# Kernel optimization log

Hardware: AMD Instinct MI355X
Metric: run time of the kernel (lower is better)

The kernel has to match this reference:

```python
import math
import jax, jax.numpy as jnp
import numpy as np

HEAD = 16
DIM = 1024
DH = DIM // HEAD
NEG = -100000000.0


def setup_inputs() -> dict:
    key = jax.random.key(0)
    ks = jax.random.split(key, 12)
    B, S, D = 2, 2048, DIM
    s = 1.0 / math.sqrt(D)
    return {
        "key": jax.random.normal(ks[0], (B, S, D), jnp.float32),
        "value": jax.random.normal(ks[1], (B, S, D), jnp.float32),
        "query": jax.random.normal(ks[2], (B, S, D), jnp.float32),
        "mask": jax.random.randint(ks[3], (B, 1, S, S), 0, 2) == 1,
        "Wq": jax.random.normal(ks[4], (D, D), jnp.float32) * s,
        "bq": jnp.zeros((D,), jnp.float32),
        "Wk": jax.random.normal(ks[5], (D, D), jnp.float32) * s,
        "bk": jnp.zeros((D,), jnp.float32),
        "Wv": jax.random.normal(ks[6], (D, D), jnp.float32) * s,
        "bv": jnp.zeros((D,), jnp.float32),
        "Wo": jax.random.normal(ks[7], (D, D), jnp.float32) * s,
        "bo": jnp.zeros((D,), jnp.float32),
    }


def _split_heads(x, b):
    # [B, S, D] -> [B, H, S, Dh]
    return x.reshape(b, -1, HEAD, DH).transpose(0, 2, 1, 3)


def reference(key, value, query, mask, Wq, bq, Wk, bk, Wv, bv, Wo, bo):
    b, k_len, d = key.shape
    q_len = query.shape[1]
    k_up = _split_heads(key @ Wk.T + bk, b)
    v_up = _split_heads(value @ Wv.T + bv, b)
    q_up = _split_heads(query @ Wq.T + bq, b) / math.sqrt(DH)
    scores = jnp.einsum("bhqd,bhkd->bhqk", q_up, k_up)
    scores = jnp.where(mask, NEG, scores)
    attn = jax.nn.softmax(scores, axis=-1)
    # dropout is identity in eval/reference mode
    context = jnp.einsum("bhqk,bhkd->bhqd", attn, v_up)
    context = context.transpose(0, 2, 1, 3).reshape(b, q_len, d)
    out = context @ Wo.T + bo
    return out, attn
```

## Files before the change

### kernel.cpp

```cpp
#include <hip/hip_runtime.h>
#include <stdint.h>

#define S_LEN 2048
#define D_MODEL 1024
#define N_HEAD 16
#define D_HEAD 64
#define N_BATCH 2
#define M_TOK (N_BATCH * S_LEN)

typedef unsigned short u16;
typedef unsigned int u32;
typedef __attribute__((ext_vector_type(8))) short bf16x8;
typedef __attribute__((ext_vector_type(4))) short s16x4;
typedef __attribute__((ext_vector_type(4))) float f32x4;
typedef __attribute__((ext_vector_type(4))) unsigned short u16x4;

#define MFMA16(a, b, c) __builtin_amdgcn_mfma_f32_16x16x32_bf16((a), (b), (c), 0, 0, 0)

#if defined(__has_builtin)
#if __has_builtin(__builtin_amdgcn_mfma_f32_16x16x16bf16_1k)
#define HAVE_MFMA_16x16x16 1
#define MFMA_PV(a, b, c) __builtin_amdgcn_mfma_f32_16x16x16bf16_1k((a), (b), (c), 0, 0, 0)
#endif
#endif

#define WAITCNT(n) asm volatile("s_waitcnt vmcnt(" #n ")" ::: "memory")
#define BAR() __builtin_amdgcn_s_barrier()

__device__ __forceinline__ u16 f2bf(float f) {
  unsigned int u = __float_as_uint(f);
  u = (u + 0x7FFFu + ((u >> 16) & 1u)) >> 16;
  return (u16)u;
}

__device__ __forceinline__ void gload_lds16(const u16* g, u16* l) {
  __builtin_amdgcn_global_load_lds((const __attribute__((address_space(1))) void*)g,
                                   (__attribute__((address_space(3))) void*)l, 16, 0, 0);
}

#define N4BIG (M_TOK * D_MODEL / 4)
#define N4W (D_MODEL * D_MODEL / 4)
__global__ __launch_bounds__(256) void cvt7_kernel(
    const float* __restrict__ sk, const float* __restrict__ sv, const float* __restrict__ sq,
    const float* __restrict__ swq, const float* __restrict__ swk, const float* __restrict__ swv,
    const float* __restrict__ swo, u16* __restrict__ dk, u16* __restrict__ dv, u16* __restrict__ dq,
    u16* __restrict__ dwq, u16* __restrict__ dwk, u16* __restrict__ dwv, u16* __restrict__ dwo) {
  const float* s;
  u16* d;
  int n4;
  switch (blockIdx.y) {
    case 0: s = sk; d = dk; n4 = N4BIG; break;
    case 1: s = sv; d = dv; n4 = N4BIG; break;
    case 2: s = sq; d = dq; n4 = N4BIG; break;
    case 3: s = swq; d = dwq; n4 = N4W; break;
    case 4: s = swk; d = dwk; n4 = N4W; break;
    case 5: s = swv; d = dwv; n4 = N4W; break;
    default: s = swo; d = dwo; n4 = N4W; break;
  }
  int i = blockIdx.x * blockDim.x + threadIdx.x;
  int stride = gridDim.x * blockDim.x;
  for (; i < n4; i += stride) {
    float4 v = ((const float4*)s)[i];
    u16x4 o = {f2bf(v.x), f2bf(v.y), f2bf(v.z), f2bf(v.w)};
    ((u16x4*)d)[i] = o;
  }
}

__global__ __launch_bounds__(256) void pack_mask(const int* __restrict__ mask,
                                                 unsigned long long* __restrict__ packed) {
  int wid = (blockIdx.x * blockDim.x + threadIdx.x) >> 6;
  int lane = threadIdx.x & 63;
  int nw = (gridDim.x * blockDim.x) >> 6;
  const int NW64 = M_TOK * (S_LEN / 64);
  for (int widx = wid; widx < NW64; widx += nw) {
    int m = mask[(size_t)widx * 64 + lane];
    unsigned long long bits = __ballot(m != 0);
    if (lane == 0) packed[widx] = bits;
  }
}

__device__ __forceinline__ void gemm_body(const u16* __restrict__ A, const u16* __restrict__ Bw,
                                          const float* __restrict__ bias, void* __restrict__ Cout,
                                          float scale, int outmode) {
  __shared__ u16 As[128 * 32];
  __shared__ u16 Bs[128 * 32];
  const int K = D_MODEL, N = D_MODEL;
  int tid = threadIdx.x;
  int w = tid >> 6, lane = tid & 63, lg = lane >> 4, lr = lane & 15;
  int m0 = blockIdx.x * 128, n0 = blockIdx.y * 128;
  int wr = w >> 1, wc = w & 1;
  f32x4 acc[4][4] = {};
  int r0 = tid >> 2;
  int r1 = 64 + (tid >> 2);
  int kk0 = (tid & 3) * 8;
  for (int kb = 0; kb < K; kb += 32) {
    gload_lds16(A + (size_t)(m0 + r0) * K + kb + kk0, As + w * 512);
    gload_lds16(A + (size_t)(m0 + r1) * K + kb + kk0, As + 2048 + w * 512);
    gload_lds16(Bw + (size_t)(n0 + r0) * K + kb + kk0, Bs + w * 512);
    gload_lds16(Bw + (size_t)(n0 + r1) * K + kb + kk0, Bs + 2048 + w * 512);
    __syncthreads();
    bf16x8 af[4], bfr[4];
#pragma unroll
    for (int i = 0; i < 4; i++)
      af[i] = *(const bf16x8*)(As + (wr * 64 + i * 16 + lr) * 32 + lg * 8);
#pragma unroll
    for (int i = 0; i < 4; i++)
      bfr[i] = *(const bf16x8*)(Bs + (wc * 64 + i * 16 + lr) * 32 + lg * 8);
#pragma unroll
    for (int mi = 0; mi < 4; mi++)
#pragma unroll
      for (int ni = 0; ni < 4; ni++)
        acc[mi][ni] = MFMA16(af[mi], bfr[ni], acc[mi][ni]);
    __syncthreads();
  }
#pragma unroll
  for (int mi = 0; mi < 4; mi++)
#pragma unroll
    for (int ni = 0; ni < 4; ni++) {
      int col = n0 + wc * 64 + ni * 16 + lr;
      float bv = bias[col];
      if (outmode == 2) {
        int row0 = m0 + wr * 64 + mi * 16 + lg * 4;
        int bb = row0 >> 11, ss = row0 & (S_LEN - 1);
        u16x4 pk;
#pragma unroll
        for (int r = 0; r < 4; r++) pk[r] = f2bf((acc[mi][ni][r] + bv) * scale);
        *(u16x4*)((u16*)Cout + ((size_t)((bb * N_HEAD + (col >> 6)) * D_HEAD + (col & 63)) * S_LEN + ss)) = pk;
      } else {
#pragma unroll
        for (int r = 0; r < 4; r++) {
          int row = m0 + wr * 64 + mi * 16 + lg * 4 + r;
          float v = (acc[mi][ni][r] + bv) * scale;
          if (outmode == 1)
            ((float*)Cout)[(size_t)row * N + col] = v;
          else
            ((u16*)Cout)[(size_t)row * N + col] = f2bf(v);
        }
      }
    }
}

#define QSCALE 0.18033688011112042f

__global__ __launch_bounds__(256) void proj3_kernel(
    const u16* __restrict__ kbf, const u16* __restrict__ vbf, const u16* __restrict__ qbf,
    const u16* __restrict__ wkb, const u16* __restrict__ wvb, const u16* __restrict__ wqb,
    const float* __restrict__ bk, const float* __restrict__ bv, const float* __restrict__ bq,
    u16* __restrict__ kup, u16* __restrict__ vtg, u16* __restrict__ qup) {
  int z = blockIdx.z;
  if (z == 0)
    gemm_body(kbf, wkb, bk, kup, 1.0f, 0);
  else if (z == 1)
    gemm_body(vbf, wvb, bv, vtg, 1.0f, 2);
  else
    gemm_body(qbf, wqb, bq, qup, QSCALE, 0);
}

__global__ __launch_bounds__(256) void gemm_out_kernel(const u16* __restrict__ A,
                                                       const u16* __restrict__ Bw,
// ... 16 lines not shown
  int h = (logical >> 6) & 15;
  int b = logical >> 10;
  int q0 = qb * 64;
  int q = q0 + w * 16 + lr;
  const float NEGV = -100000000.0f;

  bf16x8 qf0, qf1;
  {
    const u16* qrow = Qup + (size_t)(b * S_LEN + q) * D_MODEL + h * D_HEAD;
    qf0 = *(const bf16x8*)(qrow + lg * 8);
    qf1 = *(const bf16x8*)(qrow + 32 + lg * 8);
  }
  const u16* Kb = Kup + (size_t)(b * S_LEN) * D_MODEL + h * D_HEAD;
  const u32* mrow = mpack + (size_t)(b * S_LEN + q) * (S_LEN / 32) + khalf * 32;

  int srow = tid >> 3;
  int schunk = (tid & 7) ^ (srow & 7);
  const u16* KgA = Kb + (size_t)(khalf * 1024 + srow) * D_MODEL + schunk * 8;
  const int sw = lr & 7;

#define STAGE_K0(bn, ktn)                                                   \
  do {                                                                      \
    const u16* _s = KgA + (size_t)(ktn) * 64 * D_MODEL;                     \
    gload_lds16(_s, &kbuf[bn][0] + w * 512);                                \
    gload_lds16(_s + (size_t)32 * D_MODEL, &kbuf[bn][2048] + w * 512);      \
  } while (0)

  float lsA = 0.f, lsB = 0.f;
#define P0_BODY(BN, MM)                                                     \
  {                                                                         \
    const u16* kc = &kbuf[BN][0];                                           \
    _Pragma("unroll") for (int t = 0; t < 4; t++) {                         \
      const u16* kr = kc + (t * 16 + lr) * 64;                              \
      bf16x8 k0 = *(const bf16x8*)(kr + ((lg ^ sw) << 3));                  \
      bf16x8 k1 = *(const bf16x8*)(kr + (((lg + 4) ^ sw) << 3));            \
      f32x4 a = {0.f, 0.f, 0.f, 0.f};                                       \
      a = MFMA16(k0, qf0, a);                                               \
      a = MFMA16(k1, qf1, a);                                               \
      u32 wbits = (t < 2) ? (MM).x : (MM).y;                                \
      _Pragma("unroll") for (int r = 0; r < 4; r++) {                       \
        int j = (t * 16 + lg * 4 + r) & 31;                                 \
        float s = ((wbits >> j) & 1u) ? NEGV : a[r];                        \
        if (r & 1) lsB += exp2f(s); else lsA += exp2f(s);                   \
      }                                                                     \
    }                                                                       \
  }

  uint2 mA, mB;
  mA = *(const uint2*)(mrow);
  STAGE_K0(0, 0);
  for (int it = 0; it < 7; it++) {
    int kt = it * 2;
    mB = *(const uint2*)(mrow + (kt + 1) * 2);
    STAGE_K0(1, kt + 1);
    WAITCNT(3);
    BAR();
    P0_BODY(0, mA);
    BAR();
    mA = *(const uint2*)(mrow + (kt + 2) * 2);
    STAGE_K0(0, kt + 2);
    WAITCNT(3);
    BAR();
    P0_BODY(1, mB);
    BAR();
  }
  mB = *(const uint2*)(mrow + 15 * 2);
  STAGE_K0(1, 15);
  WAITCNT(3);
  BAR();
  P0_BODY(0, mA);
  BAR();
  WAITCNT(0);
  BAR();
  P0_BODY(1, mB);

  float lsum = lsA + lsB;
  lsum += __shfl_xor(lsum, 16);
  lsum += __shfl_xor(lsum, 32);
  if (lg == 0) lsums[(size_t)khalf * 65536 + (size_t)(b * N_HEAD + h) * S_LEN + q] = lsum;
#undef STAGE_K0
#undef P0_BODY
}

__global__ __launch_bounds__(512, 4) void attn_p1(
    const u16* __restrict__ Qup, const u16* __restrict__ Kup, const u16* __restrict__ Vt,
    const u32* __restrict__ mpack, const float* __restrict__ lsums,
    float* __restrict__ attn_out, u16* __restrict__ ctx) {
  __shared__ u16 kbuf[2][64 * 64];
  __shared__ u16 vbuf[2][64 * 64];
  __shared__ float pbuf[8][16][68];
  int tid = threadIdx.x;
  int w = tid >> 6, lane = tid & 63, lg = lane >> 4, lr = lane & 15;
  int fb = blockIdx.x;
  int logical = (fb & 7) * 64 + (fb >> 3);
  int qx = logical & 15;
  int h = (logical >> 4) & 15;
  int b = logical >> 8;
  int q0 = qx * 128;
  int q = q0 + w * 16 + lr;
  const float NEGV = -100000000.0f;

  bf16x8 qf0, qf1;
  {
    const u16* qrow = Qup + (size_t)(b * S_LEN + q) * D_MODEL + h * D_HEAD;
    qf0 = *(const bf16x8*)(qrow + lg * 8);
    qf1 = *(const bf16x8*)(qrow + 32 + lg * 8);
  }
  const u16* Kb = Kup + (size_t)(b * S_LEN) * D_MODEL + h * D_HEAD;
  const u16* Vb = Vt + (size_t)(b * N_HEAD + h) * D_HEAD * S_LEN;
  const u32* mrow = mpack + (size_t)(b * S_LEN + q) * (S_LEN / 32);
  float* attn_w = attn_out + ((size_t)(b * N_HEAD + h) * S_LEN + q0 + w * 16) * S_LEN;

  float il2;
  {
    size_t idx = (size_t)(b * N_HEAD + h) * S_LEN + q;
    float tot = lsums[idx] + lsums[65536 + idx];
    il2 = tot > 0.f ? -__log2f(tot) : 0.f;
  }

  int srow = tid >> 3;
  int schunk = (tid & 7) ^ (srow & 7);
  const u16* KgA = Kb + (size_t)srow * D_MODEL + schunk * 8;
  const u16* VgA = Vb + (size_t)srow * S_LEN + schunk * 8;
  const int sw = lr & 7;

#define SK(bn, ktn) gload_lds16(KgA + (size_t)(ktn) * 64 * D_MODEL, &kbuf[bn][w * 512])
#define SV(bn, ktn) gload_lds16(VgA + (size_t)(ktn) * 64, &vbuf[bn][w * 512])

  f32x4 ctxacc[4] = {};

#if defined(HAVE_MFMA_16x16x16)
#define PV_STEP(vc, t)                                                      \
  {                                                                         \
    s16x4 ap = {(short)pb[0], (short)pb[1], (short)pb[2], (short)pb[3]};    \
    _Pragma("unroll") for (int d = 0; d < 4; d++) {                         \
      s16x4 vf = *(const s16x4*)((vc) + (d * 16 + lr) * 64 +                \
                                 ((((t)*2 + (lg >> 1)) ^ sw) << 3) +        \
                                 ((lg & 1) << 2));                          \
      ctxacc[d] = MFMA_PV(ap, vf, ctxacc[d]);                               \
    }                                                                       \
  }
#else
#define PV_STEP(vc, t) (void)pb;
#endif

#define P1_BODY(BN, MM, KT)                                                 \
  {                                                                         \
    const u16* kc = &kbuf[BN][0];                                           \
    const u16* vc = &vbuf[BN][0];                                           \
    float* pw = &pbuf[w][0][0];                                             \
    _Pragma("unroll") for (int t = 0; t < 4; t++) {                         \
      const u16* kr = kc + (t * 16 + lr) * 64;                              \
      bf16x8 k0 = *(const bf16x8*)(kr + ((lg ^ sw) << 3));                  \
      bf16x8 k1 = *(const bf16x8*)(kr + (((lg + 4) ^ sw) << 3));            \
      f32x4 a = {0.f, 0.f, 0.f, 0.f};                                       \
      a = MFMA16(k0, qf0, a);                                               \
      a = MFMA16(k1, qf1, a);                                               \
      u32 wbits = (t < 2) ? (MM).x : (MM).y;                                \
      f32x4 p;                                                              \
      u16x4 pb;                                                             \
      _Pragma("unroll") for (int r = 0; r < 4; r++) {                       \
        int j = (t * 16 + lg * 4 + r) & 31;                                 \
        float s = ((wbits >> j) & 1u) ? NEGV : (a[r] + il2);                \
        float pv = exp2f(s);                                                \
        p[r] = pv;                                                          \
        pb[r] = f2bf(pv);                                                   \
      }                                                                     \
      *(f32x4*)(pw + lr * 68 + t * 16 + lg * 4) = p;                        \
      PV_STEP(vc, t)                                                        \
    }                                                                       \
                    \
    P1_FALLBACK_PV(vc)                                                      \
             \
    _Pragma("unroll") for (int i = 0; i < 4; i++) {                         \
      int rl = (lane >> 4) + i * 4;                                         \
      int cc = lane & 15;                                                   \
      f32x4 v = *(const f32x4*)(&pbuf[w][0][0] + rl * 68 + cc * 4);         \
      *(f32x4*)(attn_w + (size_t)rl * S_LEN + (KT) * 64 + cc * 4) = v;      \
    }                                                                       \
  }

#if defined(HAVE_MFMA_16x16x16)
#define P1_FALLBACK_PV(vc)
#else
#define P1_FALLBACK_PV(vc)                                                  \
  {                                                                         \
    float* pw = &pbuf[w][0][0];                                             \
    bf16x8 pa0, pa1;                                                        \
    _Pragma("unroll") for (int e = 0; e < 8; e++) {                         \
      pa0[e] = (short)f2bf(pw[lr * 68 + lg * 8 + e]);                       \
      pa1[e] = (short)f2bf(pw[lr * 68 + 32 + lg * 8 + e]);                  \
    }                                                                       \
    _Pragma("unroll") for (int d = 0; d < 4; d++) {                         \
      const u16* vr = (vc) + (d * 16 + lr) * 64;                            \
      bf16x8 v0 = *(const bf16x8*)(vr + ((lg ^ sw) << 3));                  \
      bf16x8 v1 = *(const bf16x8*)(vr + (((lg + 4) ^ sw) << 3));            \
      ctxacc[d] = MFMA16(pa0, v0, ctxacc[d]);                               \
      ctxacc[d] = MFMA16(pa1, v1, ctxacc[d]);                               \
    }                                                                       \
  }
#endif

  uint2 mA, mB;
  mA = *(const uint2*)(mrow);
  SK(0, 0);
  SV(0, 0);
  mB = *(const uint2*)(mrow + 1 * 2);
  SK(1, 1);
  SV(1, 1);
  WAITCNT(3);
  BAR();
  P1_BODY(0, mA, 0);
  BAR();
  mA = *(const uint2*)(mrow + 2 * 2);
  SK(0, 2);
  SV(0, 2);
  WAITCNT(7);
  BAR();
  P1_BODY(1, mB, 1);
  BAR();
  for (int it = 1; it < 15; it++) {
    int kt = it * 2;
    mB = *(const uint2*)(mrow + (kt + 1) * 2);
    SK(1, kt + 1);
    SV(1, kt + 1);
    WAITCNT(7);
    BAR();
    P1_BODY(0, mA, kt);
    BAR();
    mA = *(const uint2*)(mrow + (kt + 2) * 2);
    SK(0, kt + 2);
    SV(0, kt + 2);
    WAITCNT(7);
    BAR();
    P1_BODY(1, mB, kt + 1);
    BAR();
  }
  mB = *(const uint2*)(mrow + 31 * 2);
  SK(1, 31);
  SV(1, 31);
  WAITCNT(7);
  BAR();
  P1_BODY(0, mA, 30);
  BAR();
  WAITCNT(4);
  BAR();
  P1_BODY(1, mB, 31);

#pragma unroll
  for (int d = 0; d < 4; d++)
#pragma unroll
    for (int r = 0; r < 4; r++) {
      int sq = q0 + w * 16 + lg * 4 + r;
      ctx[(size_t)(b * S_LEN + sq) * D_MODEL + h * D_HEAD + d * 16 + lr] = f2bf(ctxacc[d][r]);
    }
#undef SK
#undef SV
#undef P1_BODY
#undef PV_STEP
#undef P1_FALLBACK_PV
}

#define O_KBF 0u
#define O_VBF 4194304u
#define O_QBF 8388608u
#define O_WQ 12582912u
#define O_WK 13631488u
#define O_WV 14680064u
#define O_WO 15728640u
#define O_QUP 16777216u
#define O_KUP 20971520u
#define O_VUP 25165824u
#define O_CTX 29360128u

extern "C" void kernel_launch(void* const* d_in, const int* in_sizes, int n_in,
                              void* d_out, int out_size, void* d_ws, size_t ws_size,
                              hipStream_t stream) {
  const float* key = (const float*)d_in[0];
  const float* value = (const float*)d_in[1];
  const float* query = (const float*)d_in[2];
  const int* mask = (const int*)d_in[3];
  const float* Wq = (const float*)d_in[4];
  const float* bq = (const float*)d_in[5];
  const float* Wk = (const float*)d_in[6];
  const float* bk = (const float*)d_in[7];
  const float* Wv = (const float*)d_in[8];
  const float* bv = (const float*)d_in[9];
  const float* Wo = (const float*)d_in[10];
  const float* bo = (const float*)d_in[11];

  u16* ws = (u16*)d_ws;
  u16* kbf = ws + O_KBF;
  u16* vbf = ws + O_VBF;
  u16* qbf = ws + O_QBF;
  u16* wqb = ws + O_WQ;
  u16* wkb = ws + O_WK;
  u16* wvb = ws + O_WV;
  u16* wob = ws + O_WO;
  u16* qup = ws + O_QUP;
  u16* kup = ws + O_KUP;
  u16* vtg = ws + O_VUP;
  u16* ctxb = ws + O_CTX;
  float* lsums = (float*)(ws + O_VBF);

  float* out = (float*)d_out;
  float* attn = out + (size_t)N_BATCH * S_LEN * D_MODEL;

  cvt7_kernel<<<dim3(512, 7), 256, 0, stream>>>(key, value, query, Wq, Wk, Wv, Wo, kbf, vbf, qbf,
                                                wqb, wkb, wvb, wob);
  proj3_kernel<<<dim3(32, 8, 3), 256, 0, stream>>>(kbf, vbf, qbf, wkb, wvb, wqb, bk, bv, bq, kup,
                                                   vtg, qup);
  pack_mask<<<1024, 256, 0, stream>>>(mask, (unsigned long long*)kbf);
  attn_p0<<<2048, 256, 0, stream>>>(qup, kup, (const u32*)kbf, lsums);
  attn_p1<<<512, 512, 0, stream>>>(qup, kup, vtg, (const u32*)kbf, lsums, attn, ctxb);
  gemm_out_kernel<<<dim3(32, 8), 256, 0, stream>>>(ctxb, wob, bo, out);
}
```

Baseline: 333.8 us.

## Split attention pass over key halves, stream attn directly, reduce context separately

The second attention pass now uses 256-thread blocks covering 64 queries and half of the key range, so four times as many blocks launch with a higher occupancy hint. Probabilities go straight to global memory instead of through a shared-memory staging buffer, and V fragments are read directly from global rather than staged in LDS. The two partial fp32 context results are written to scratch space (one of them in the output buffer before the final GEMM overwrites it) and combined by a new reduce kernel. This adds an extra kernel plus fp32 partial traffic, and the direct attn stores are narrower and less coalesced.

```diff
diff --git a/kernel.cpp b/kernel.cpp
--- a/kernel.cpp
+++ b/kernel.cpp
@@ -10,6 +10,7 @@
 
 typedef unsigned short u16;
 typedef unsigned int u32;
+typedef unsigned long long u64;
 typedef __attribute__((ext_vector_type(8))) short bf16x8;
 typedef __attribute__((ext_vector_type(4))) short s16x4;
 typedef __attribute__((ext_vector_type(4))) float f32x4;
@@ -67,14 +68,14 @@
 }
 
 __global__ __launch_bounds__(256) void pack_mask(const int* __restrict__ mask,
-                                                 unsigned long long* __restrict__ packed) {
+                                                 u64* __restrict__ packed) {
   int wid = (blockIdx.x * blockDim.x + threadIdx.x) >> 6;
   int lane = threadIdx.x & 63;
   int nw = (gridDim.x * blockDim.x) >> 6;
   const int NW64 = M_TOK * (S_LEN / 64);
   for (int widx = wid; widx < NW64; widx += nw) {
     int m = mask[(size_t)widx * 64 + lane];
-    unsigned long long bits = __ballot(m != 0);
+    u64 bits = __ballot(m != 0);
     if (lane == 0) packed[widx] = bits;
   }
 }
@@ -257,21 +258,23 @@
 #undef P0_BODY
 }
 
-__global__ __launch_bounds__(512, 4) void attn_p1(
+__global__ __launch_bounds__(256, 6) void attn_p1(
     const u16* __restrict__ Qup, const u16* __restrict__ Kup, const u16* __restrict__ Vt,
     const u32* __restrict__ mpack, const float* __restrict__ lsums,
-    float* __restrict__ attn_out, u16* __restrict__ ctx) {
+    float* __restrict__ attn_out, float* __restrict__ ctx0, float* __restrict__ ctx1) {
   __shared__ u16 kbuf[2][64 * 64];
-  __shared__ u16 vbuf[2][64 * 64];
-  __shared__ float pbuf[8][16][68];
+#if !defined(HAVE_MFMA_16x16x16)
+  __shared__ u16 pbuf[4][16 * 64];
+#endif
   int tid = threadIdx.x;
   int w = tid >> 6, lane = tid & 63, lg = lane >> 4, lr = lane & 15;
   int fb = blockIdx.x;
-  int logical = (fb & 7) * 64 + (fb >> 3);
-  int qx = logical & 15;
-  int h = (logical >> 4) & 15;
-  int b = logical >> 8;
-  int q0 = qx * 128;
+  int logical = (fb & 7) * 256 + (fb >> 3);
+  int khalf = logical & 1;
+  int qb = (logical >> 1) & 31;
+  int h = (logical >> 6) & 15;
+  int b = logical >> 10;
+  int q0 = qb * 64;
   int q = q0 + w * 16 + lr;
   const float NEGV = -100000000.0f;
 
@@ -282,9 +285,9 @@
     qf1 = *(const bf16x8*)(qrow + 32 + lg * 8);
   }
   const u16* Kb = Kup + (size_t)(b * S_LEN) * D_MODEL + h * D_HEAD;
-  const u16* Vb = Vt + (size_t)(b * N_HEAD + h) * D_HEAD * S_LEN;
-  const u32* mrow = mpack + (size_t)(b * S_LEN + q) * (S_LEN / 32);
-  float* attn_w = attn_out + ((size_t)(b * N_HEAD + h) * S_LEN + q0 + w * 16) * S_LEN;
+  const u16* Vb = Vt + (size_t)(b * N_HEAD + h) * D_HEAD * S_LEN + khalf * 1024;
+  const u32* mrow = mpack + (size_t)(b * S_LEN + q) * (S_LEN / 32) + khalf * 32;
+  float* attn_b = attn_out + ((size_t)(b * N_HEAD + h) * S_LEN + q) * S_LEN + khalf * 1024;
 
   float il2;
   {
@@ -295,35 +298,23 @@
 
   int srow = tid >> 3;
   int schunk = (tid & 7) ^ (srow & 7);
-  const u16* KgA = Kb + (size_t)srow * D_MODEL + schunk * 8;
-  const u16* VgA = Vb + (size_t)srow * S_LEN + schunk * 8;
+  const u16* KgA = Kb + (size_t)(khalf * 1024 + srow) * D_MODEL + schunk * 8;
   const int sw = lr & 7;
 
-#define SK(bn, ktn) gload_lds16(KgA + (size_t)(ktn) * 64 * D_MODEL, &kbuf[bn][w * 512])
-#define SV(bn, ktn) gload_lds16(VgA + (size_t)(ktn) * 64, &vbuf[bn][w * 512])
+#define STAGE_K1(bn, ktn)                                                   \
+  do {                                                                      \
+    const u16* _s = KgA + (size_t)(ktn) * 64 * D_MODEL;                     \
+    gload_lds16(_s, &kbuf[bn][0] + w * 512);                                \
+    gload_lds16(_s + (size_t)32 * D_MODEL, &kbuf[bn][2048] + w * 512);      \
+  } while (0)
 
   f32x4 ctxacc[4] = {};
 
 #if defined(HAVE_MFMA_16x16x16)
-#define PV_STEP(vc, t)                                                      \
-  {                                                                         \
-    s16x4 ap = {(short)pb[0], (short)pb[1], (short)pb[2], (short)pb[3]};    \
-    _Pragma("unroll") for (int d = 0; d < 4; d++) {                         \
-      s16x4 vf = *(const s16x4*)((vc) + (d * 16 + lr) * 64 +                \
-                                 ((((t)*2 + (lg >> 1)) ^ sw) << 3) +        \
-                                 ((lg & 1) << 2));                          \
-      ctxacc[d] = MFMA_PV(ap, vf, ctxacc[d]);                               \
-    }                                                                       \
-  }
-#else
-#define PV_STEP(vc, t) (void)pb;
-#endif
-
 #define P1_BODY(BN, MM, KT)                                                 \
   {                                                                         \
     const u16* kc = &kbuf[BN][0];                                           \
-    const u16* vc = &vbuf[BN][0];                                           \
-    float* pw = &pbuf[w][0][0];                                             \
+    const u16* vg = Vb + (KT) * 64;                                         \
     _Pragma("unroll") for (int t = 0; t < 4; t++) {                         \
       const u16* kr = kc + (t * 16 + lr) * 64;                              \
       bf16x8 k0 = *(const bf16x8*)(kr + ((lg ^ sw) << 3));                  \
@@ -341,35 +332,48 @@
         p[r] = pv;                                                          \
         pb[r] = f2bf(pv);                                                   \
       }                                                                     \
-      *(f32x4*)(pw + lr * 68 + t * 16 + lg * 4) = p;                        \
-      PV_STEP(vc, t)                                                        \
+      *(f32x4*)(attn_b + (KT) * 64 + t * 16 + lg * 4) = p;                  \
+      s16x4 ap = {(short)pb[0], (short)pb[1], (short)pb[2], (short)pb[3]};  \
+      _Pragma("unroll") for (int d = 0; d < 4; d++) {                       \
+        s16x4 vf = *(const s16x4*)(vg + (size_t)(d * 16 + lr) * S_LEN +     \
+                                   t * 16 + lg * 4);                        \
+        ctxacc[d] = MFMA_PV(ap, vf, ctxacc[d]);                             \
+      }                                                                     \
     }                                                                       \
-                    \
-    P1_FALLBACK_PV(vc)                                                      \
-             \
-    _Pragma("unroll") for (int i = 0; i < 4; i++) {                         \
-      int rl = (lane >> 4) + i * 4;                                         \
-      int cc = lane & 15;                                                   \
-      f32x4 v = *(const f32x4*)(&pbuf[w][0][0] + rl * 68 + cc * 4);         \
-      *(f32x4*)(attn_w + (size_t)rl * S_LEN + (KT) * 64 + cc * 4) = v;      \
+  }
+#else
+#define P1_BODY(BN, MM, KT)                                                 \
+  {                                                                         \
+    const u16* kc = &kbuf[BN][0];                                           \
+    const u16* vg = Vb + (KT) * 64;                                         \
+    u16* pw = &pbuf[w][0];                                                  \
+    _Pragma("unroll") for (int t = 0; t < 4; t++) {                         \
+      const u16* kr = kc + (t * 16 + lr) * 64;                              \
+      bf16x8 k0 = *(const bf16x8*)(kr + ((lg ^ sw) << 3));                  \
+      bf16x8 k1 = *(const bf16x8*)(kr + (((lg + 4) ^ sw) << 3));            \
+      f32x4 a = {0.f, 0.f, 0.f, 0.f};                                       \
+      a = MFMA16(k0, qf0, a);                                               \
+      a = MFMA16(k1, qf1, a);                                               \
+      u32 wbits = (t < 2) ? (MM).x : (MM).y;                                \
+      f32x4 p;                                                              \
+      u16x4 pb;                                                             \
+      _Pragma("unroll") for (int r = 0; r < 4; r++) {                       \
+        int j = (t * 16 + lg * 4 + r) & 31;                                 \
+        float s = ((wbits >> j) & 1u) ? NEGV : (a[r] + il2);                \
+        float pv = exp2f(s);                                                \
+        p[r] = pv;                                                          \
+        pb[r] = f2bf(pv);                                                   \
+      }                                                                     \
+      *(f32x4*)(attn_b + (KT) * 64 + t * 16 + lg * 4) = p;                  \
+      *(u16x4*)(pw + lr * 64 + (((t * 2 + (lg >> 1)) ^ sw) << 3) +          \
+                ((lg & 1) << 2)) = pb;                                      \
     }                                                                       \
-  }
-
-#if defined(HAVE_MFMA_16x16x16)
-#define P1_FALLBACK_PV(vc)
-#else
-#define P1_FALLBACK_PV(vc)                                                  \
-  {                                                                         \
-    float* pw = &pbuf[w][0][0];                                             \
-    bf16x8 pa0, pa1;                                                        \
-    _Pragma("unroll") for (int e = 0; e < 8; e++) {                         \
-      pa0[e] = (short)f2bf(pw[lr * 68 + lg * 8 + e]);                       \
-      pa1[e] = (short)f2bf(pw[lr * 68 + 32 + lg * 8 + e]);                  \
-    }                                                                       \
+    bf16x8 pa0 = *(const bf16x8*)(pw + lr * 64 + ((lg ^ sw) << 3));         \
+    bf16x8 pa1 = *(const bf16x8*)(pw + lr * 64 + (((lg + 4) ^ sw) << 3));   \
     _Pragma("unroll") for (int d = 0; d < 4; d++) {                         \
-      const u16* vr = (vc) + (d * 16 + lr) * 64;                            \
-      bf16x8 v0 = *(const bf16x8*)(vr + ((lg ^ sw) << 3));                  \
-      bf16x8 v1 = *(const bf16x8*)(vr + (((lg + 4) ^ sw) << 3));            \
+      const u16* vr = vg + (size_t)(d * 16 + lr) * S_LEN;                   \
+      bf16x8 v0 = *(const bf16x8*)(vr + lg * 8);                            \
+      bf16x8 v1 = *(const bf16x8*)(vr + 32 + lg * 8);                       \
       ctxacc[d] = MFMA16(pa0, v0, ctxacc[d]);                               \
       ctxacc[d] = MFMA16(pa1, v1, ctxacc[d]);                               \
     }                                                                       \
@@ -378,62 +382,52 @@
 
   uint2 mA, mB;
   mA = *(const uint2*)(mrow);
-  SK(0, 0);
-  SV(0, 0);
-  mB = *(const uint2*)(mrow + 1 * 2);
-  SK(1, 1);
-  SV(1, 1);
-  WAITCNT(3);
-  BAR();
-  P1_BODY(0, mA, 0);
-  BAR();
-  mA = *(const uint2*)(mrow + 2 * 2);
-  SK(0, 2);
-  SV(0, 2);
-  WAITCNT(7);
-  BAR();
-  P1_BODY(1, mB, 1);
-  BAR();
-  for (int it = 1; it < 15; it++) {
+  STAGE_K1(0, 0);
+  for (int it = 0; it < 7; it++) {
     int kt = it * 2;
     mB = *(const uint2*)(mrow + (kt + 1) * 2);
-    SK(1, kt + 1);
-    SV(1, kt + 1);
-    WAITCNT(7);
+    STAGE_K1(1, kt + 1);
+    WAITCNT(3);
     BAR();
     P1_BODY(0, mA, kt);
     BAR();
     mA = *(const uint2*)(mrow + (kt + 2) * 2);
-    SK(0, kt + 2);
-    SV(0, kt + 2);
-    WAITCNT(7);
+    STAGE_K1(0, kt + 2);
+    WAITCNT(3);
     BAR();
     P1_BODY(1, mB, kt + 1);
     BAR();
   }
-  mB = *(const uint2*)(mrow + 31 * 2);
-  SK(1, 31);
-  SV(1, 31);
-  WAITCNT(7);
-  BAR();
-  P1_BODY(0, mA, 30);
-  BAR();
-  WAITCNT(4);
-  BAR();
-  P1_BODY(1, mB, 31);
-
+  mB = *(const uint2*)(mrow + 15 * 2);
+  STAGE_K1(1, 15);
+  WAITCNT(3);
+  BAR();
+  P1_BODY(0, mA, 14);
+  BAR();
+  WAITCNT(0);
+  BAR();
+  P1_BODY(1, mB, 15);
+
+  float* cdst = khalf ? ctx1 : ctx0;
 #pragma unroll
   for (int d = 0; d < 4; d++)
 #pragma unroll
     for (int r = 0; r < 4; r++) {
       int sq = q0 + w * 16 + lg * 4 + r;
-      ctx[(size_t)(b * S_LEN + sq) * D_MODEL + h * D_HEAD + d * 16 + lr] = f2bf(ctxacc[d][r]);
+      cdst[(size_t)(b * S_LEN + sq) * D_MODEL + h * D_HEAD + d * 16 + lr] = ctxacc[d][r];
     }
-#undef SK
-#undef SV
+#undef STAGE_K1
 #undef P1_BODY
-#undef PV_STEP
-#undef P1_FALLBACK_PV
+}
+
+__global__ __launch_bounds__(256) void ctx_reduce(const float* __restrict__ c0,
+                                                  const float* __restrict__ c1,
+                                                  u16* __restrict__ dst) {
+  int i = blockIdx.x * 256 + threadIdx.x;
+  f32x4 a = ((const f32x4*)c0)[i];
+  f32x4 bv = ((const f32x4*)c1)[i];
+  u16x4 o = {f2bf(a[0] + bv[0]), f2bf(a[1] + bv[1]), f2bf(a[2] + bv[2]), f2bf(a[3] + bv[3])};
+  ((u16x4*)dst)[i] = o;
 }
 
 #define O_KBF 0u
@@ -476,17 +470,21 @@
   u16* kup = ws + O_KUP;
   u16* vtg = ws + O_VUP;
   u16* ctxb = ws + O_CTX;
-  float* lsums = (float*)(ws + O_VBF);
+  u64* maskp = (u64*)(ws + O_CTX);
+  float* lsums = (float*)(ws + O_CTX + 524288);
+  float* ctx0 = (float*)(ws + O_KBF);
 
   float* out = (float*)d_out;
   float* attn = out + (size_t)N_BATCH * S_LEN * D_MODEL;
+  float* ctx1 = out;
 
   cvt7_kernel<<<dim3(512, 7), 256, 0, stream>>>(key, value, query, Wq, Wk, Wv, Wo, kbf, vbf, qbf,
                                                 wqb, wkb, wvb, wob);
   proj3_kernel<<<dim3(32, 8, 3), 256, 0, stream>>>(kbf, vbf, qbf, wkb, wvb, wqb, bk, bv, bq, kup,
                                                    vtg, qup);
-  pack_mask<<<1024, 256, 0, stream>>>(mask, (unsigned long long*)kbf);
-  attn_p0<<<2048, 256, 0, stream>>>(qup, kup, (const u32*)kbf, lsums);
-  attn_p1<<<512, 512, 0, stream>>>(qup, kup, vtg, (const u32*)kbf, lsums, attn, ctxb);
+  pack_mask<<<1024, 256, 0, stream>>>(mask, maskp);
+  attn_p0<<<2048, 256, 0, stream>>>(qup, kup, (const u32*)maskp, lsums);
+  attn_p1<<<2048, 256, 0, stream>>>(qup, kup, vtg, (const u32*)maskp, lsums, attn, ctx0, ctx1);
+  ctx_reduce<<<4096, 256, 0, stream>>>(ctx0, ctx1, ctxb);
   gemm_out_kernel<<<dim3(32, 8), 256, 0, stream>>>(ctxb, wob, bo, out);
 }
```

New measurement: 558.4 us. +67.3%, slower.

## Split attn_p1 keys across two wave halves, write attn directly, reduce context in LDS

Applied to the files above, without the earlier changes.

The attention second pass now has each 512-thread block cover 64 queries instead of 128. The block's two 4-wave halves each take half of the key range with smaller 32-key tiles, and their partial context sums are added through LDS at the end. The attention probabilities are stored straight from registers to global memory instead of being staged through a per-wave LDS buffer. Together with the grid doubling to 1024 blocks and launch bounds raised to 8, this aims for more occupancy and parallelism, at the cost of narrower, less coalesced attn stores and an extra reduction step.

```diff
diff --git a/kernel.cpp b/kernel.cpp
--- a/kernel.cpp
+++ b/kernel.cpp
@@ -10,6 +10,7 @@
 
 typedef unsigned short u16;
 typedef unsigned int u32;
+typedef unsigned long long u64;
 typedef __attribute__((ext_vector_type(8))) short bf16x8;
 typedef __attribute__((ext_vector_type(4))) short s16x4;
 typedef __attribute__((ext_vector_type(4))) float f32x4;
@@ -67,14 +68,14 @@
 }
 
 __global__ __launch_bounds__(256) void pack_mask(const int* __restrict__ mask,
-                                                 unsigned long long* __restrict__ packed) {
+                                                 u64* __restrict__ packed) {
   int wid = (blockIdx.x * blockDim.x + threadIdx.x) >> 6;
   int lane = threadIdx.x & 63;
   int nw = (gridDim.x * blockDim.x) >> 6;
   const int NW64 = M_TOK * (S_LEN / 64);
   for (int widx = wid; widx < NW64; widx += nw) {
     int m = mask[(size_t)widx * 64 + lane];
-    unsigned long long bits = __ballot(m != 0);
+    u64 bits = __ballot(m != 0);
     if (lane == 0) packed[widx] = bits;
   }
 }
@@ -257,22 +258,25 @@
 #undef P0_BODY
 }
 
-__global__ __launch_bounds__(512, 4) void attn_p1(
+__global__ __launch_bounds__(512, 8) void attn_p1(
     const u16* __restrict__ Qup, const u16* __restrict__ Kup, const u16* __restrict__ Vt,
     const u32* __restrict__ mpack, const float* __restrict__ lsums,
     float* __restrict__ attn_out, u16* __restrict__ ctx) {
-  __shared__ u16 kbuf[2][64 * 64];
-  __shared__ u16 vbuf[2][64 * 64];
-  __shared__ float pbuf[8][16][68];
+  __shared__ u16 kbuf[2][2][32 * 64];
+  __shared__ u16 vbuf[2][2][64 * 32];
+#if !defined(HAVE_MFMA_16x16x16)
+  __shared__ u16 pbuf[8][16 * 32];
+#endif
   int tid = threadIdx.x;
   int w = tid >> 6, lane = tid & 63, lg = lane >> 4, lr = lane & 15;
+  int half = w >> 2, band = w & 3;
   int fb = blockIdx.x;
-  int logical = (fb & 7) * 64 + (fb >> 3);
-  int qx = logical & 15;
-  int h = (logical >> 4) & 15;
-  int b = logical >> 8;
-  int q0 = qx * 128;
-  int q = q0 + w * 16 + lr;
+  int logical = (fb & 7) * 128 + (fb >> 3);
+  int qx = logical & 31;
+  int h = (logical >> 5) & 15;
+  int b = logical >> 9;
+  int q0 = qx * 64;
+  int q = q0 + band * 16 + lr;
   const float NEGV = -100000000.0f;
 
   bf16x8 qf0, qf1;
@@ -283,8 +287,8 @@
   }
   const u16* Kb = Kup + (size_t)(b * S_LEN) * D_MODEL + h * D_HEAD;
   const u16* Vb = Vt + (size_t)(b * N_HEAD + h) * D_HEAD * S_LEN;
-  const u32* mrow = mpack + (size_t)(b * S_LEN + q) * (S_LEN / 32);
-  float* attn_w = attn_out + ((size_t)(b * N_HEAD + h) * S_LEN + q0 + w * 16) * S_LEN;
+  const u32* mrow = mpack + (size_t)(b * S_LEN + q) * (S_LEN / 32) + half * 32;
+  float* attn_b = attn_out + ((size_t)(b * N_HEAD + h) * S_LEN + q) * S_LEN + half * 1024;
 
   float il2;
   {
@@ -293,147 +297,156 @@
     il2 = tot > 0.f ? -__log2f(tot) : 0.f;
   }
 
-  int srow = tid >> 3;
+  int lt = tid & 255;
+  int srow = lt >> 3;
   int schunk = (tid & 7) ^ (srow & 7);
-  const u16* KgA = Kb + (size_t)srow * D_MODEL + schunk * 8;
-  const u16* VgA = Vb + (size_t)srow * S_LEN + schunk * 8;
-  const int sw = lr & 7;
-
-#define SK(bn, ktn) gload_lds16(KgA + (size_t)(ktn) * 64 * D_MODEL, &kbuf[bn][w * 512])
-#define SV(bn, ktn) gload_lds16(VgA + (size_t)(ktn) * 64, &vbuf[bn][w * 512])
+  const u16* KgA = Kb + (size_t)(half * 1024 + srow) * D_MODEL + schunk * 8;
+  int vrow = lt >> 2;
+  int vchunk = (tid & 3) ^ (vrow & 3);
+  const u16* VgA = Vb + (size_t)vrow * S_LEN + half * 1024 + vchunk * 8;
+  const int swk = lr & 7;
+  const int swv = lr & 3;
+
+#define SK(bn, ktn) gload_lds16(KgA + (size_t)(ktn) * 32 * D_MODEL, &kbuf[half][bn][(w & 3) * 512])
+#define SV(bn, ktn) gload_lds16(VgA + (size_t)(ktn) * 32, &vbuf[half][bn][(w & 3) * 512])
 
   f32x4 ctxacc[4] = {};
 
 #if defined(HAVE_MFMA_16x16x16)
-#define PV_STEP(vc, t)                                                      \
-  {                                                                         \
-    s16x4 ap = {(short)pb[0], (short)pb[1], (short)pb[2], (short)pb[3]};    \
-    _Pragma("unroll") for (int d = 0; d < 4; d++) {                         \
-      s16x4 vf = *(const s16x4*)((vc) + (d * 16 + lr) * 64 +                \
-                                 ((((t)*2 + (lg >> 1)) ^ sw) << 3) +        \
-                                 ((lg & 1) << 2));                          \
-      ctxacc[d] = MFMA_PV(ap, vf, ctxacc[d]);                               \
-    }                                                                       \
-  }
-#else
-#define PV_STEP(vc, t) (void)pb;
-#endif
-
 #define P1_BODY(BN, MM, KT)                                                 \
   {                                                                         \
-    const u16* kc = &kbuf[BN][0];                                           \
-    const u16* vc = &vbuf[BN][0];                                           \
-    float* pw = &pbuf[w][0][0];                                             \
-    _Pragma("unroll") for (int t = 0; t < 4; t++) {                         \
+    const u16* kc = &kbuf[half][BN][0];                                     \
+    const u16* vc = &vbuf[half][BN][0];                                     \
+    _Pragma("unroll") for (int t = 0; t < 2; t++) {                         \
       const u16* kr = kc + (t * 16 + lr) * 64;                              \
-      bf16x8 k0 = *(const bf16x8*)(kr + ((lg ^ sw) << 3));                  \
-      bf16x8 k1 = *(const bf16x8*)(kr + (((lg + 4) ^ sw) << 3));            \
+      bf16x8 k0 = *(const bf16x8*)(kr + ((lg ^ swk) << 3));                 \
+      bf16x8 k1 = *(const bf16x8*)(kr + (((lg + 4) ^ swk) << 3));           \
       f32x4 a = {0.f, 0.f, 0.f, 0.f};                                       \
       a = MFMA16(k0, qf0, a);                                               \
       a = MFMA16(k1, qf1, a);                                               \
-      u32 wbits = (t < 2) ? (MM).x : (MM).y;                                \
       f32x4 p;                                                              \
       u16x4 pb;                                                             \
       _Pragma("unroll") for (int r = 0; r < 4; r++) {                       \
-        int j = (t * 16 + lg * 4 + r) & 31;                                 \
-        float s = ((wbits >> j) & 1u) ? NEGV : (a[r] + il2);                \
+        int j = t * 16 + lg * 4 + r;                                        \
+        float s = (((MM) >> j) & 1u) ? NEGV : (a[r] + il2);                 \
         float pv = exp2f(s);                                                \
         p[r] = pv;                                                          \
         pb[r] = f2bf(pv);                                                   \
       }                                                                     \
-      *(f32x4*)(pw + lr * 68 + t * 16 + lg * 4) = p;                        \
-      PV_STEP(vc, t)                                                        \
+      *(f32x4*)(attn_b + (KT) * 32 + t * 16 + lg * 4) = p;                  \
+      s16x4 ap = {(short)pb[0], (short)pb[1], (short)pb[2], (short)pb[3]};  \
+      _Pragma("unroll") for (int d = 0; d < 4; d++) {                       \
+        s16x4 vf = *(const s16x4*)(vc + (d * 16 + lr) * 32 +                \
+                                   (((t * 2 + (lg >> 1)) ^ swv) << 3) +     \
+                                   ((lg & 1) << 2));                        \
+        ctxacc[d] = MFMA_PV(ap, vf, ctxacc[d]);                             \
+      }                                                                     \
     }                                                                       \
-                    \
-    P1_FALLBACK_PV(vc)                                                      \
-             \
-    _Pragma("unroll") for (int i = 0; i < 4; i++) {                         \
-      int rl = (lane >> 4) + i * 4;                                         \
-      int cc = lane & 15;                                                   \
-      f32x4 v = *(const f32x4*)(&pbuf[w][0][0] + rl * 68 + cc * 4);         \
-      *(f32x4*)(attn_w + (size_t)rl * S_LEN + (KT) * 64 + cc * 4) = v;      \
+  }
+#else
+#define P1_BODY(BN, MM, KT)                                                 \
+  {                                                                         \
+    const u16* kc = &kbuf[half][BN][0];                                     \
+    const u16* vc = &vbuf[half][BN][0];                                     \
+    u16* pw = &pbuf[w][0];                                                  \
+    _Pragma("unroll") for (int t = 0; t < 2; t++) {                         \
+      const u16* kr = kc + (t * 16 + lr) * 64;                              \
+      bf16x8 k0 = *(const bf16x8*)(kr + ((lg ^ swk) << 3));                 \
+      bf16x8 k1 = *(const bf16x8*)(kr + (((lg + 4) ^ swk) << 3));           \
+      f32x4 a = {0.f, 0.f, 0.f, 0.f};                                       \
+      a = MFMA16(k0, qf0, a);                                               \
+      a = MFMA16(k1, qf1, a);                                               \
+      f32x4 p;                                                              \
+      u16x4 pb;                                                             \
+      _Pragma("unroll") for (int r = 0; r < 4; r++) {                       \
+        int j = t * 16 + lg * 4 + r;                                        \
+        float s = (((MM) >> j) & 1u) ? NEGV : (a[r] + il2);                 \
+        float pv = exp2f(s);                                                \
+        p[r] = pv;                                                          \
+        pb[r] = f2bf(pv);                                                   \
+      }                                                                     \
+      *(f32x4*)(attn_b + (KT) * 32 + t * 16 + lg * 4) = p;                  \
+      *(u16x4*)(pw + lr * 32 + (((t * 2 + (lg >> 1)) ^ swv) << 3) +         \
+                ((lg & 1) << 2)) = pb;                                      \
     }                                                                       \
-  }
-
-#if defined(HAVE_MFMA_16x16x16)
-#define P1_FALLBACK_PV(vc)
-#else
-#define P1_FALLBACK_PV(vc)                                                  \
-  {                                                                         \
-    float* pw = &pbuf[w][0][0];                                             \
-    bf16x8 pa0, pa1;                                                        \
-    _Pragma("unroll") for (int e = 0; e < 8; e++) {                         \
-      pa0[e] = (short)f2bf(pw[lr * 68 + lg * 8 + e]);                       \
-      pa1[e] = (short)f2bf(pw[lr * 68 + 32 + lg * 8 + e]);                  \
+    bf16x8 pa = *(const bf16x8*)(pw + lr * 32 + ((lg ^ swv) << 3));         \
+    _Pragma("unroll") for (int d = 0; d < 4; d++) {                         \
+      bf16x8 v0 = *(const bf16x8*)(vc + (d * 16 + lr) * 32 +                \
+                                   ((lg ^ swv) << 3));                      \
+      ctxacc[d] = MFMA16(pa, v0, ctxacc[d]);                                \
     }                                                                       \
-    _Pragma("unroll") for (int d = 0; d < 4; d++) {                         \
-      const u16* vr = (vc) + (d * 16 + lr) * 64;                            \
-      bf16x8 v0 = *(const bf16x8*)(vr + ((lg ^ sw) << 3));                  \
-      bf16x8 v1 = *(const bf16x8*)(vr + (((lg + 4) ^ sw) << 3));            \
-      ctxacc[d] = MFMA16(pa0, v0, ctxacc[d]);                               \
-      ctxacc[d] = MFMA16(pa1, v1, ctxacc[d]);                               \
-    }                                                                       \
   }
 #endif
 
-  uint2 mA, mB;
-  mA = *(const uint2*)(mrow);
+  u32 mA, mB;
+  mA = mrow[0];
   SK(0, 0);
   SV(0, 0);
-  mB = *(const uint2*)(mrow + 1 * 2);
+  mB = mrow[1];
   SK(1, 1);
   SV(1, 1);
   WAITCNT(3);
   BAR();
   P1_BODY(0, mA, 0);
   BAR();
-  mA = *(const uint2*)(mrow + 2 * 2);
+  mA = mrow[2];
   SK(0, 2);
   SV(0, 2);
-  WAITCNT(7);
+  WAITCNT(5);
   BAR();
   P1_BODY(1, mB, 1);
   BAR();
   for (int it = 1; it < 15; it++) {
     int kt = it * 2;
-    mB = *(const uint2*)(mrow + (kt + 1) * 2);
+    mB = mrow[kt + 1];
     SK(1, kt + 1);
     SV(1, kt + 1);
-    WAITCNT(7);
+    WAITCNT(5);
     BAR();
     P1_BODY(0, mA, kt);
     BAR();
-    mA = *(const uint2*)(mrow + (kt + 2) * 2);
+    mA = mrow[kt + 2];
     SK(0, kt + 2);
     SV(0, kt + 2);
-    WAITCNT(7);
+    WAITCNT(5);
     BAR();
     P1_BODY(1, mB, kt + 1);
     BAR();
   }
-  mB = *(const uint2*)(mrow + 31 * 2);
+  mB = mrow[31];
   SK(1, 31);
   SV(1, 31);
-  WAITCNT(7);
+  WAITCNT(5);
   BAR();
   P1_BODY(0, mA, 30);
   BAR();
-  WAITCNT(4);
+  WAITCNT(2);
   BAR();
   P1_BODY(1, mB, 31);
 
-#pragma unroll
-  for (int d = 0; d < 4; d++)
-#pragma unroll
-    for (int r = 0; r < 4; r++) {
-      int sq = q0 + w * 16 + lg * 4 + r;
-      ctx[(size_t)(b * S_LEN + sq) * D_MODEL + h * D_HEAD + d * 16 + lr] = f2bf(ctxacc[d][r]);
-    }
+  __syncthreads();
+  float* red = (float*)&kbuf[0][0][0];
+  if (half == 1) {
+#pragma unroll
+    for (int d = 0; d < 4; d++)
+#pragma unroll
+      for (int r = 0; r < 4; r++)
+        red[(band * 16 + lg * 4 + r) * 64 + d * 16 + lr] = ctxacc[d][r];
+  }
+  __syncthreads();
+  if (half == 0) {
+#pragma unroll
+    for (int d = 0; d < 4; d++)
+#pragma unroll
+      for (int r = 0; r < 4; r++) {
+        int ql = band * 16 + lg * 4 + r;
+        float v = ctxacc[d][r] + red[ql * 64 + d * 16 + lr];
+        ctx[(size_t)(b * S_LEN + q0 + ql) * D_MODEL + h * D_HEAD + d * 16 + lr] = f2bf(v);
+      }
+  }
 #undef SK
 #undef SV
 #undef P1_BODY
-#undef PV_STEP
-#undef P1_FALLBACK_PV
 }
 
 #define O_KBF 0u
@@ -476,7 +489,8 @@
   u16* kup = ws + O_KUP;
   u16* vtg = ws + O_VUP;
   u16* ctxb = ws + O_CTX;
-  float* lsums = (float*)(ws + O_VBF);
+  u64* maskp = (u64*)kbf;
+  float* lsums = (float*)vbf;
 
   float* out = (float*)d_out;
   float* attn = out + (size_t)N_BATCH * S_LEN * D_MODEL;
@@ -485,8 +499,8 @@
                                                 wqb, wkb, wvb, wob);
   proj3_kernel<<<dim3(32, 8, 3), 256, 0, stream>>>(kbf, vbf, qbf, wkb, wvb, wqb, bk, bv, bq, kup,
                                                    vtg, qup);
-  pack_mask<<<1024, 256, 0, stream>>>(mask, (unsigned long long*)kbf);
-  attn_p0<<<2048, 256, 0, stream>>>(qup, kup, (const u32*)kbf, lsums);
-  attn_p1<<<512, 512, 0, stream>>>(qup, kup, vtg, (const u32*)kbf, lsums, attn, ctxb);
+  pack_mask<<<1024, 256, 0, stream>>>(mask, maskp);
+  attn_p0<<<2048, 256, 0, stream>>>(qup, kup, (const u32*)maskp, lsums);
+  attn_p1<<<1024, 512, 0, stream>>>(qup, kup, vtg, (const u32*)maskp, lsums, attn, ctxb);
   gemm_out_kernel<<<dim3(32, 8), 256, 0, stream>>>(ctxb, wob, bo, out);
 }
```

New measurement: 520.0 us. 1.56x slower.

## Write attention probabilities straight from registers and shrink attn_p1 blocks to 64 queries

Applied to the files above, without the earlier changes.

attn_p1 no longer stages probabilities through a padded fp32 LDS buffer before storing them. Each lane now writes its four fp32 values directly to global memory, which removes the LDS round trip and the extra copy loop. Blocks go from 512 to 256 threads covering 64 queries each, launched as a 1024-block grid with launch bounds of 5, and each wave issues two K/V async loads per tile, so the waitcnt values change to match. The direct stores are only 16 bytes per lane spread across many rows, so global write coalescing gets worse, and each K/V tile is now loaded once per 64 queries instead of once per 128.

```diff
diff --git a/kernel.cpp b/kernel.cpp
--- a/kernel.cpp
+++ b/kernel.cpp
@@ -10,6 +10,7 @@
 
 typedef unsigned short u16;
 typedef unsigned int u32;
+typedef unsigned long long u64;
 typedef __attribute__((ext_vector_type(8))) short bf16x8;
 typedef __attribute__((ext_vector_type(4))) short s16x4;
 typedef __attribute__((ext_vector_type(4))) float f32x4;
@@ -67,14 +68,14 @@
 }
 
 __global__ __launch_bounds__(256) void pack_mask(const int* __restrict__ mask,
-                                                 unsigned long long* __restrict__ packed) {
+                                                 u64* __restrict__ packed) {
   int wid = (blockIdx.x * blockDim.x + threadIdx.x) >> 6;
   int lane = threadIdx.x & 63;
   int nw = (gridDim.x * blockDim.x) >> 6;
   const int NW64 = M_TOK * (S_LEN / 64);
   for (int widx = wid; widx < NW64; widx += nw) {
     int m = mask[(size_t)widx * 64 + lane];
-    unsigned long long bits = __ballot(m != 0);
+    u64 bits = __ballot(m != 0);
     if (lane == 0) packed[widx] = bits;
   }
 }
@@ -257,21 +258,23 @@
 #undef P0_BODY
 }
 
-__global__ __launch_bounds__(512, 4) void attn_p1(
+__global__ __launch_bounds__(256, 5) void attn_p1(
     const u16* __restrict__ Qup, const u16* __restrict__ Kup, const u16* __restrict__ Vt,
     const u32* __restrict__ mpack, const float* __restrict__ lsums,
     float* __restrict__ attn_out, u16* __restrict__ ctx) {
   __shared__ u16 kbuf[2][64 * 64];
   __shared__ u16 vbuf[2][64 * 64];
-  __shared__ float pbuf[8][16][68];
+#if !defined(HAVE_MFMA_16x16x16)
+  __shared__ u16 pbuf[4][16 * 64];
+#endif
   int tid = threadIdx.x;
   int w = tid >> 6, lane = tid & 63, lg = lane >> 4, lr = lane & 15;
   int fb = blockIdx.x;
-  int logical = (fb & 7) * 64 + (fb >> 3);
-  int qx = logical & 15;
-  int h = (logical >> 4) & 15;
-  int b = logical >> 8;
-  int q0 = qx * 128;
+  int logical = (fb & 7) * 128 + (fb >> 3);
+  int qx = logical & 31;
+  int h = (logical >> 5) & 15;
+  int b = logical >> 9;
+  int q0 = qx * 64;
   int q = q0 + w * 16 + lr;
   const float NEGV = -100000000.0f;
 
@@ -284,7 +287,7 @@
   const u16* Kb = Kup + (size_t)(b * S_LEN) * D_MODEL + h * D_HEAD;
   const u16* Vb = Vt + (size_t)(b * N_HEAD + h) * D_HEAD * S_LEN;
   const u32* mrow = mpack + (size_t)(b * S_LEN + q) * (S_LEN / 32);
-  float* attn_w = attn_out + ((size_t)(b * N_HEAD + h) * S_LEN + q0 + w * 16) * S_LEN;
+  float* attn_b = attn_out + ((size_t)(b * N_HEAD + h) * S_LEN + q) * S_LEN;
 
   float il2;
   {
@@ -299,80 +302,89 @@
   const u16* VgA = Vb + (size_t)srow * S_LEN + schunk * 8;
   const int sw = lr & 7;
 
-#define SK(bn, ktn) gload_lds16(KgA + (size_t)(ktn) * 64 * D_MODEL, &kbuf[bn][w * 512])
-#define SV(bn, ktn) gload_lds16(VgA + (size_t)(ktn) * 64, &vbuf[bn][w * 512])
+#define SK(bn, ktn)                                                          \
+  do {                                                                       \
+    const u16* _s = KgA + (size_t)(ktn) * 64 * D_MODEL;                      \
+    gload_lds16(_s, &kbuf[bn][0] + w * 512);                                 \
+    gload_lds16(_s + (size_t)32 * D_MODEL, &kbuf[bn][2048] + w * 512);       \
+  } while (0)
+#define SV(bn, ktn)                                                          \
+  do {                                                                       \
+    const u16* _s = VgA + (size_t)(ktn) * 64;                                \
+    gload_lds16(_s, &vbuf[bn][0] + w * 512);                                 \
+    gload_lds16(_s + (size_t)32 * S_LEN, &vbuf[bn][2048] + w * 512);         \
+  } while (0)
 
   f32x4 ctxacc[4] = {};
 
 #if defined(HAVE_MFMA_16x16x16)
-#define PV_STEP(vc, t)                                                      \
-  {                                                                         \
-    s16x4 ap = {(short)pb[0], (short)pb[1], (short)pb[2], (short)pb[3]};    \
-    _Pragma("unroll") for (int d = 0; d < 4; d++) {                         \
-      s16x4 vf = *(const s16x4*)((vc) + (d * 16 + lr) * 64 +                \
-                                 ((((t)*2 + (lg >> 1)) ^ sw) << 3) +        \
-                                 ((lg & 1) << 2));                          \
-      ctxacc[d] = MFMA_PV(ap, vf, ctxacc[d]);                               \
-    }                                                                       \
+#define P1_BODY(BN, MM, KT)                                                  \
+  {                                                                          \
+    const u16* kc = &kbuf[BN][0];                                            \
+    const u16* vc = &vbuf[BN][0];                                            \
+    _Pragma("unroll") for (int t = 0; t < 4; t++) {                          \
+      const u16* kr = kc + (t * 16 + lr) * 64;                               \
+      bf16x8 k0 = *(const bf16x8*)(kr + ((lg ^ sw) << 3));                   \
+      bf16x8 k1 = *(const bf16x8*)(kr + (((lg + 4) ^ sw) << 3));             \
+      f32x4 a = {0.f, 0.f, 0.f, 0.f};                                        \
+      a = MFMA16(k0, qf0, a);                                                \
+      a = MFMA16(k1, qf1, a);                                                \
+      u32 wbits = (t < 2) ? (MM).x : (MM).y;                                 \
+      f32x4 p;                                                               \
+      u16x4 pb;                                                              \
+      _Pragma("unroll") for (int r = 0; r < 4; r++) {                        \
+        int j = (t * 16 + lg * 4 + r) & 31;                                  \
+        float s = ((wbits >> j) & 1u) ? NEGV : (a[r] + il2);                 \
+        float pv = exp2f(s);                                                 \
+        p[r] = pv;                                                           \
+        pb[r] = f2bf(pv);                                                    \
+      }                                                                      \
+      *(f32x4*)(attn_b + (KT) * 64 + t * 16 + lg * 4) = p;                   \
+      s16x4 ap = {(short)pb[0], (short)pb[1], (short)pb[2], (short)pb[3]};   \
+      _Pragma("unroll") for (int d = 0; d < 4; d++) {                        \
+        s16x4 vf = *(const s16x4*)(vc + (d * 16 + lr) * 64 +                 \
+                                   (((t * 2 + (lg >> 1)) ^ sw) << 3) +       \
+                                   ((lg & 1) << 2));                         \
+        ctxacc[d] = MFMA_PV(ap, vf, ctxacc[d]);                              \
+      }                                                                      \
+    }                                                                        \
   }
 #else
-#define PV_STEP(vc, t) (void)pb;
-#endif
-
-#define P1_BODY(BN, MM, KT)                                                 \
-  {                                                                         \
-    const u16* kc = &kbuf[BN][0];                                           \
-    const u16* vc = &vbuf[BN][0];                                           \
-    float* pw = &pbuf[w][0][0];                                             \
-    _Pragma("unroll") for (int t = 0; t < 4; t++) {                         \
-      const u16* kr = kc + (t * 16 + lr) * 64;                              \
-      bf16x8 k0 = *(const bf16x8*)(kr + ((lg ^ sw) << 3));                  \
-      bf16x8 k1 = *(const bf16x8*)(kr + (((lg + 4) ^ sw) << 3));            \
-      f32x4 a = {0.f, 0.f, 0.f, 0.f};                                       \
-      a = MFMA16(k0, qf0, a);                                               \
-      a = MFMA16(k1, qf1, a);                                               \
-      u32 wbits = (t < 2) ? (MM).x : (MM).y;                                \
-      f32x4 p;                                                              \
-      u16x4 pb;                                                             \
-      _Pragma("unroll") for (int r = 0; r < 4; r++) {                       \
-        int j = (t * 16 + lg * 4 + r) & 31;                                 \
-        float s = ((wbits >> j) & 1u) ? NEGV : (a[r] + il2);                \
-        float pv = exp2f(s);                                                \
-        p[r] = pv;                                                          \
-        pb[r] = f2bf(pv);                                                   \
-      }                                                                     \
-      *(f32x4*)(pw + lr * 68 + t * 16 + lg * 4) = p;                        \
-      PV_STEP(vc, t)                                                        \
-    }                                                                       \
-                    \
-    P1_FALLBACK_PV(vc)                                                      \
-             \
-    _Pragma("unroll") for (int i = 0; i < 4; i++) {                         \
-      int rl = (lane >> 4) + i * 4;                                         \
-      int cc = lane & 15;                                                   \
-      f32x4 v = *(const f32x4*)(&pbuf[w][0][0] + rl * 68 + cc * 4);         \
-      *(f32x4*)(attn_w + (size_t)rl * S_LEN + (KT) * 64 + cc * 4) = v;      \
-    }                                                                       \
-  }
-
-#if defined(HAVE_MFMA_16x16x16)
-#define P1_FALLBACK_PV(vc)
-#else
-#define P1_FALLBACK_PV(vc)                                                  \
-  {                                                                         \
-    float* pw = &pbuf[w][0][0];                                             \
-    bf16x8 pa0, pa1;                                                        \
-    _Pragma("unroll") for (int e = 0; e < 8; e++) {                         \
-      pa0[e] = (short)f2bf(pw[lr * 68 + lg * 8 + e]);                       \
-      pa1[e] = (short)f2bf(pw[lr * 68 + 32 + lg * 8 + e]);                  \
-    }                                                                       \
-    _Pragma("unroll") for (int d = 0; d < 4; d++) {                         \
-      const u16* vr = (vc) + (d * 16 + lr) * 64;                            \
-      bf16x8 v0 = *(const bf16x8*)(vr + ((lg ^ sw) << 3));                  \
-      bf16x8 v1 = *(const bf16x8*)(vr + (((lg + 4) ^ sw) << 3));            \
-      ctxacc[d] = MFMA16(pa0, v0, ctxacc[d]);                               \
-      ctxacc[d] = MFMA16(pa1, v1, ctxacc[d]);                               \
-    }                                                                       \
+#define P1_BODY(BN, MM, KT)                                                  \
+  {                                                                          \
+    const u16* kc = &kbuf[BN][0];                                            \
+    const u16* vc = &vbuf[BN][0];                                            \
+    u16* pw = &pbuf[w][0];                                                   \
+    _Pragma("unroll") for (int t = 0; t < 4; t++) {                          \
+      const u16* kr = kc + (t * 16 + lr) * 64;                               \
+      bf16x8 k0 = *(const bf16x8*)(kr + ((lg ^ sw) << 3));                   \
+      bf16x8 k1 = *(const bf16x8*)(kr + (((lg + 4) ^ sw) << 3));             \
+      f32x4 a = {0.f, 0.f, 0.f, 0.f};                                        \
+      a = MFMA16(k0, qf0, a);                                                \
+      a = MFMA16(k1, qf1, a);                                                \
+      u32 wbits = (t < 2) ? (MM).x : (MM).y;                                 \
+      f32x4 p;                                                               \
+      u16x4 pb;                                                              \
+      _Pragma("unroll") for (int r = 0; r < 4; r++) {                        \
+        int j = (t * 16 + lg * 4 + r) & 31;                                  \
+        float s = ((wbits >> j) & 1u) ? NEGV : (a[r] + il2);                 \
+        float pv = exp2f(s);                                                 \
+        p[r] = pv;                                                           \
+        pb[r] = f2bf(pv);                                                    \
+      }                                                                      \
+      *(f32x4*)(attn_b + (KT) * 64 + t * 16 + lg * 4) = p;                   \
+      *(u16x4*)(pw + lr * 64 + (((t * 2 + (lg >> 1)) ^ sw) << 3) +           \
+                ((lg & 1) << 2)) = pb;                                       \
+    }                                                                        \
+    bf16x8 pa0 = *(const bf16x8*)(pw + lr * 64 + ((lg ^ sw) << 3));          \
+    bf16x8 pa1 = *(const bf16x8*)(pw + lr * 64 + (((lg + 4) ^ sw) << 3));    \
+    _Pragma("unroll") for (int d = 0; d < 4; d++) {                          \
+      const u16* vr = vc + (d * 16 + lr) * 64;                               \
+      bf16x8 v0 = *(const bf16x8*)(vr + ((lg ^ sw) << 3));                   \
+      bf16x8 v1 = *(const bf16x8*)(vr + (((lg + 4) ^ sw) << 3));             \
+      ctxacc[d] = MFMA16(pa0, v0, ctxacc[d]);                                \
+      ctxacc[d] = MFMA16(pa1, v1, ctxacc[d]);                                \
+    }                                                                        \
   }
 #endif
 
@@ -383,14 +395,14 @@
   mB = *(const uint2*)(mrow + 1 * 2);
   SK(1, 1);
   SV(1, 1);
-  WAITCNT(3);
+  WAITCNT(5);
   BAR();
   P1_BODY(0, mA, 0);
   BAR();
   mA = *(const uint2*)(mrow + 2 * 2);
   SK(0, 2);
   SV(0, 2);
-  WAITCNT(7);
+  WAITCNT(9);
   BAR();
   P1_BODY(1, mB, 1);
   BAR();
@@ -399,14 +411,14 @@
     mB = *(const uint2*)(mrow + (kt + 1) * 2);
     SK(1, kt + 1);
     SV(1, kt + 1);
-    WAITCNT(7);
+    WAITCNT(9);
     BAR();
     P1_BODY(0, mA, kt);
     BAR();
     mA = *(const uint2*)(mrow + (kt + 2) * 2);
     SK(0, kt + 2);
     SV(0, kt + 2);
-    WAITCNT(7);
+    WAITCNT(9);
     BAR();
     P1_BODY(1, mB, kt + 1);
     BAR();
@@ -414,7 +426,7 @@
   mB = *(const uint2*)(mrow + 31 * 2);
   SK(1, 31);
   SV(1, 31);
-  WAITCNT(7);
+  WAITCNT(9);
   BAR();
   P1_BODY(0, mA, 30);
   BAR();
@@ -432,8 +444,6 @@
 #undef SK
 #undef SV
 #undef P1_BODY
-#undef PV_STEP
-#undef P1_FALLBACK_PV
 }
 
 #define O_KBF 0u
@@ -476,7 +486,8 @@
   u16* kup = ws + O_KUP;
   u16* vtg = ws + O_VUP;
   u16* ctxb = ws + O_CTX;
-  float* lsums = (float*)(ws + O_VBF);
+  u64* maskp = (u64*)kbf;
+  float* lsums = (float*)vbf;
 
   float* out = (float*)d_out;
   float* attn = out + (size_t)N_BATCH * S_LEN * D_MODEL;
@@ -485,8 +496,8 @@
                                                 wqb, wkb, wvb, wob);
   proj3_kernel<<<dim3(32, 8, 3), 256, 0, stream>>>(kbf, vbf, qbf, wkb, wvb, wqb, bk, bv, bq, kup,
                                                    vtg, qup);
-  pack_mask<<<1024, 256, 0, stream>>>(mask, (unsigned long long*)kbf);
-  attn_p0<<<2048, 256, 0, stream>>>(qup, kup, (const u32*)kbf, lsums);
-  attn_p1<<<512, 512, 0, stream>>>(qup, kup, vtg, (const u32*)kbf, lsums, attn, ctxb);
+  pack_mask<<<1024, 256, 0, stream>>>(mask, maskp);
+  attn_p0<<<2048, 256, 0, stream>>>(qup, kup, (const u32*)maskp, lsums);
+  attn_p1<<<1024, 256, 0, stream>>>(qup, kup, vtg, (const u32*)maskp, lsums, attn, ctxb);
   gemm_out_kernel<<<dim3(32, 8), 256, 0, stream>>>(ctxb, wob, bo, out);
 }
```

Result: slower. 357.8 us (+7.2%).
